# Optimization experiments

Hardware: AMD Instinct MI355X
Metric: run time of the kernel (lower is better)

## Reference

```python
import jax, jax.numpy as jnp
import numpy as np

H = 8  # num heads
LORA_SCALE = 1.0


def _lora(x, down, up):
    # down: [rank, in], up: [out, rank]; sigma_mask is None -> ones -> no-op
    return (x @ down.T) @ up.T


def setup_inputs() -> dict:
    key = jax.random.key(0)
    ks = jax.random.split(key, 16)
    B, S, C = 16, 1024, 1280
    Senc, Cenc = 77, 1024
    rank = 4
    s = lambda n: 1.0 / np.sqrt(n)
    inp = {
        "hidden_states": jax.random.normal(ks[0], (B, S, C), jnp.float32),
        "encoder_hidden_states": jax.random.normal(ks[1], (B, Senc, Cenc), jnp.float32),
        "Wq": jax.random.normal(ks[2], (C, C), jnp.float32) * s(C),
        "Wk": jax.random.normal(ks[3], (C, Cenc), jnp.float32) * s(Cenc),
        "Wv": jax.random.normal(ks[4], (C, Cenc), jnp.float32) * s(Cenc),
        "Wo": jax.random.normal(ks[5], (C, C), jnp.float32) * s(C),
        "bo": jnp.zeros((C,), jnp.float32),
        "q_down": jax.random.normal(ks[6], (rank, C), jnp.float32) / rank,
        "q_up": jax.random.normal(ks[7], (C, rank), jnp.float32) * 0.02,
        "k_down": jax.random.normal(ks[8], (rank, Cenc), jnp.float32) / rank,
        "k_up": jax.random.normal(ks[9], (C, rank), jnp.float32) * 0.02,
        "v_down": jax.random.normal(ks[10], (rank, Cenc), jnp.float32) / rank,
        "v_up": jax.random.normal(ks[11], (C, rank), jnp.float32) * 0.02,
        "o_down": jax.random.normal(ks[12], (rank, C), jnp.float32) / rank,
        "o_up": jax.random.normal(ks[13], (C, rank), jnp.float32) * 0.02,
    }
    return inp


def reference(hidden_states, encoder_hidden_states, Wq, Wk, Wv, Wo, bo,
              q_down, q_up, k_down, k_up, v_down, v_up, o_down, o_up):
    B, S, C = hidden_states.shape
    Senc = encoder_hidden_states.shape[1]
    D = C // H
    attn_scale = 1.0 / jnp.sqrt(jnp.asarray(D, hidden_states.dtype))

    q = hidden_states @ Wq.T + LORA_SCALE * _lora(hidden_states, q_down, q_up)
    k = encoder_hidden_states @ Wk.T + LORA_SCALE * _lora(encoder_hidden_states, k_down, k_up)
    v = encoder_hidden_states @ Wv.T + LORA_SCALE * _lora(encoder_hidden_states, v_down, v_up)

    # head_to_batch_dim: [B, S, H*D] -> [B, H, S, D]
    q = q.reshape(B, S, H, D).transpose(0, 2, 1, 3)
    k = k.reshape(B, Senc, H, D).transpose(0, 2, 1, 3)
    v = v.reshape(B, Senc, H, D).transpose(0, 2, 1, 3)

    scores = jnp.einsum("bhqd,bhkd->bhqk", q, k) * attn_scale
    probs = jax.nn.softmax(scores, axis=-1)
    out = jnp.einsum("bhqk,bhkd->bhqd", probs, v)

    # batch_to_head_dim: [B, H, S, D] -> [B, S, H*D]
    out = out.transpose(0, 2, 1, 3).reshape(B, S, C)
    out = out @ Wo.T + bo + LORA_SCALE * _lora(out, o_down, o_up)
    return out
```

## Files before the change

kernel.cpp:

```cpp
#include <hip/hip_runtime.h>

#define NH    8
#define BB    16
#define SQ    1024
#define CC    1280
#define SENC  77
#define CENC  1024
#define DH    160
#define RANK  4

typedef __attribute__((ext_vector_type(8))) short bf16x8;
typedef __attribute__((ext_vector_type(4))) float f32x4;

__device__ inline void split_bf16(float a, unsigned short& hi, unsigned short& lo) {
    unsigned u = __float_as_uint(a);
    hi = (unsigned short)(u >> 16);
    float fhi = __uint_as_float(u & 0xffff0000u);
    float r = a - fhi;
    lo = (unsigned short)(__float_as_uint(r) >> 16);
}

__global__ void fold_split_kernel(const float* __restrict__ W,
                                  const float* __restrict__ up,
                                  const float* __restrict__ down,
                                  unsigned short* __restrict__ ohi,
                                  unsigned short* __restrict__ olo,
                                  int N, int K) {
    int idx4 = blockIdx.x * blockDim.x + threadIdx.x;
    int total4 = (N * K) >> 2;
    if (idx4 >= total4) return;
    int i = idx4 << 2;
    int n = i / K;
    int kk = i - n * K;
    float4 acc = *(const float4*)(W + i);
#pragma unroll
    for (int r = 0; r < RANK; ++r) {
        float u = up[n * RANK + r];
        float4 dv = *(const float4*)(down + (size_t)r * K + kk);
        acc.x += u * dv.x; acc.y += u * dv.y;
        acc.z += u * dv.z; acc.w += u * dv.w;
    }
    unsigned short h0, h1, h2, h3, l0, l1, l2, l3;
    split_bf16(acc.x, h0, l0); split_bf16(acc.y, h1, l1);
    split_bf16(acc.z, h2, l2); split_bf16(acc.w, h3, l3);
    int2 hv, lv;
    hv.x = (int)((unsigned)h0 | ((unsigned)h1 << 16));
    hv.y = (int)((unsigned)h2 | ((unsigned)h3 << 16));
    lv.x = (int)((unsigned)l0 | ((unsigned)l1 << 16));
    lv.y = (int)((unsigned)l2 | ((unsigned)l3 << 16));
    *(int2*)(ohi + i) = hv;
    *(int2*)(olo + i) = lv;
}

__global__ void fold_split_kv_kernel(const float* __restrict__ Wk,
                                     const float* __restrict__ Wv,
                                     const float* __restrict__ k_up,
                                     const float* __restrict__ k_down,
                                     const float* __restrict__ v_up,
                                     const float* __restrict__ v_down,
                                     unsigned short* __restrict__ ohi,
                                     unsigned short* __restrict__ olo) {
    int idx4 = blockIdx.x * blockDim.x + threadIdx.x;
    int i = idx4 << 2;
    int n = i >> 10;
    int kk = i & 1023;
    const float* W; const float* up; const float* down; int nn = n;
    if (n < CC) { W = Wk; up = k_up; down = k_down; }
    else        { W = Wv; up = v_up; down = v_down; nn = n - CC; }
    float4 acc = *(const float4*)(W + (size_t)nn * CENC + kk);
#pragma unroll
    for (int r = 0; r < RANK; ++r) {
        float u = up[nn * RANK + r];
        float4 dv = *(const float4*)(down + (size_t)r * CENC + kk);
        acc.x += u * dv.x; acc.y += u * dv.y;
        acc.z += u * dv.z; acc.w += u * dv.w;
    }
    unsigned short h0, h1, h2, h3, l0, l1, l2, l3;
    split_bf16(acc.x, h0, l0); split_bf16(acc.y, h1, l1);
    split_bf16(acc.z, h2, l2); split_bf16(acc.w, h3, l3);
    int2 hv, lv;
    hv.x = (int)((unsigned)h0 | ((unsigned)h1 << 16));
    hv.y = (int)((unsigned)h2 | ((unsigned)h3 << 16));
    lv.x = (int)((unsigned)l0 | ((unsigned)l1 << 16));
    lv.y = (int)((unsigned)l2 | ((unsigned)l3 << 16));
    *(int2*)(ohi + i) = hv;
    *(int2*)(olo + i) = lv;
}

__global__ __launch_bounds__(256) void foldT_split_kernel(
    const float* __restrict__ W, const float* __restrict__ up,
    const float* __restrict__ down,
    unsigned short* __restrict__ ohi, unsigned short* __restrict__ olo) {
    __shared__ float t[32][33];
    int tx = threadIdx.x & 31, ty = threadIdx.x >> 5;
    int bx = blockIdx.x, by = blockIdx.y;
    int k = bx * 32 + tx;
#pragma unroll
    for (int r4 = 0; r4 < 4; ++r4) {
        int n = by * 32 + ty + 8 * r4;
        float v = W[(size_t)n * 1280 + k];
#pragma unroll
        for (int r = 0; r < RANK; ++r)
            v += up[n * RANK + r] * down[r * 1280 + k];
        t[ty + 8 * r4][tx] = v;
    }
    __syncthreads();
#pragma unroll
    for (int r4 = 0; r4 < 4; ++r4) {
        float v = t[tx][ty + 8 * r4];
        unsigned short h_, l_;
        split_bf16(v, h_, l_);
        size_t o = (size_t)(bx * 32 + ty + 8 * r4) * 1280 + by * 32 + tx;
        ohi[o] = h_; olo[o] = l_;
    }
}

__global__ void split_kernel(const float* __restrict__ x,
                             unsigned short* __restrict__ ohi,
                             unsigned short* __restrict__ olo, int total4) {
    int idx4 = blockIdx.x * blockDim.x + threadIdx.x;
    if (idx4 >= total4) return;
    int i = idx4 << 2;
    float4 a = *(const float4*)(x + i);
    unsigned short h0, h1, h2, h3, l0, l1, l2, l3;
    split_bf16(a.x, h0, l0); split_bf16(a.y, h1, l1);
    split_bf16(a.z, h2, l2); split_bf16(a.w, h3, l3);
    int2 hv, lv;
    hv.x = (int)((unsigned)h0 | ((unsigned)h1 << 16));
    hv.y = (int)((unsigned)h2 | ((unsigned)h3 << 16));
    lv.x = (int)((unsigned)l0 | ((unsigned)l1 << 16));
    lv.y = (int)((unsigned)l2 | ((unsigned)l3 << 16));
    *(int2*)(ohi + i) = hv;
    *(int2*)(olo + i) = lv;
}

#define GBM 128
#define GBN 128
#define GBK 32

__device__ inline void async_load16(const void* gsrc, void* lds_dst) {
    __builtin_amdgcn_global_load_lds(
        (const __attribute__((address_space(1))) void*)gsrc,
        (__attribute__((address_space(3))) void*)lds_dst, 16, 0, 0);
}

__device__ inline int clampi(int x, int hi) { return x > hi ? hi : x; }

template <int MODE>
__global__ __launch_bounds__(256) void gemm2_kernel(
    const unsigned short* __restrict__ A_hi, const unsigned short* __restrict__ A_lo,
    int lda,
    const unsigned short* __restrict__ W_hi, const unsigned short* __restrict__ W_lo,
    int ldw,
    const float* __restrict__ bias, float* __restrict__ outF,
    unsigned short* __restrict__ oHi, unsigned short* __restrict__ oLo, int ldo,
    int M, int N, int K) {
    __shared__ __align__(16) unsigned short lds[4][GBM][GBK];
    const int tid  = threadIdx.x;
    const int wave = tid >> 6;
    const int lane = tid & 63;

    int m0, n0;
    if constexpr (MODE == 0) {
        n0 = blockIdx.x * GBN; m0 = blockIdx.y * GBM;
    } else if constexpr (MODE == 1) {
        n0 = blockIdx.x * GBN; m0 = 0;
        int z = blockIdx.z, b = z >> 3, hh = z & 7;
        size_t ao = (size_t)(b * SENC) * lda + hh * DH;
        A_hi += ao; A_lo += ao;
        W_hi += hh * DH; W_lo += hh * DH;
        size_t ob = (size_t)(b * 640 + hh * 80) * ldo;
        oHi += ob; oLo += ob;
    } else if constexpr (MODE == 2) {
        n0 = 0; m0 = blockIdx.y * GBM;
        int z = blockIdx.z, b = z >> 3, hh = z & 7;
        A_hi += hh * DH; A_lo += hh * DH;
        size_t wo = (size_t)(b * SENC) * ldw + CC + hh * DH;
        W_hi += wo; W_lo += wo;
        size_t ob = (size_t)b * CC * ldo + hh * 80;
        oHi += ob; oLo += ob;
    } else {
        int bid = blockIdx.x;
        int w = (bid & 7) * 160 + (bid >> 3);
        int mt = w / 10, nt = w - mt * 10;
        m0 = mt * GBM; n0 = nt * GBN;
        int b = m0 >> 10;
        size_t wo = (size_t)b * CC * ldw;
        W_hi += wo; W_lo += wo;
    }

    const int wr = wave >> 1, wc = wave & 1;
    f32x4 zero = {0.f, 0.f, 0.f, 0.f};
    f32x4 acc[4][4];
#pragma unroll
    for (int i = 0; i < 4; ++i)
#pragma unroll
        for (int j = 0; j < 4; ++j) acc[i][j] = zero;

    const int c0 = wave * 2, c1 = wave * 2 + 1;
    const int rr = lane >> 2;
    const int kc = (lane & 3) * 8;
    const int ra0 = clampi(m0 + c0 * 16 + rr, M - 1);
    const int ra1 = clampi(m0 + c1 * 16 + rr, M - 1);
    const int rw0 = clampi(n0 + c0 * 16 + rr, N - 1);
    const int rw1 = clampi(n0 + c1 * 16 + rr, N - 1);
    const unsigned short* pAh0 = A_hi + (size_t)ra0 * lda + kc;
    const unsigned short* pAh1 = A_hi + (size_t)ra1 * lda + kc;
    const unsigned short* pAl0 = A_lo + (size_t)ra0 * lda + kc;
    const unsigned short* pAl1 = A_lo + (size_t)ra1 * lda + kc;
    const unsigned short* pWh0 = W_hi + (size_t)rw0 * ldw + kc;
    const unsigned short* pWh1 = W_hi + (size_t)rw1 * ldw + kc;
    const unsigned short* pWl0 = W_lo + (size_t)rw0 * ldw + kc;
    const unsigned short* pWl1 = W_lo + (size_t)rw1 * ldw + kc;

    for (int k0 = 0; k0 < K; k0 += GBK) {
        async_load16(pAh0 + k0, &lds[0][c0 * 16][0]);
        async_load16(pAh1 + k0, &lds[0][c1 * 16][0]);
        async_load16(pAl0 + k0, &lds[1][c0 * 16][0]);
        async_load16(pAl1 + k0, &lds[1][c1 * 16][0]);
        async_load16(pWh0 + k0, &lds[2][c0 * 16][0]);
        async_load16(pWh1 + k0, &lds[2][c1 * 16][0]);
        async_load16(pWl0 + k0, &lds[3][c0 * 16][0]);
        async_load16(pWl1 + k0, &lds[3][c1 * 16][0]);
        __syncthreads();

        bf16x8 ah[4], al[4], bh[4], bl[4];
        const int fr = lane & 15;
        const int kb = (lane >> 4) * 8;
#pragma unroll
        for (int i = 0; i < 4; ++i) {
            ah[i] = *(const bf16x8*)&lds[0][wr * 64 + i * 16 + fr][kb];
            al[i] = *(const bf16x8*)&lds[1][wr * 64 + i * 16 + fr][kb];
            bh[i] = *(const bf16x8*)&lds[2][wc * 64 + i * 16 + fr][kb];
            bl[i] = *(const bf16x8*)&lds[3][wc * 64 + i * 16 + fr][kb];
        }
#pragma unroll
        for (int i = 0; i < 4; ++i)
#pragma unroll
            for (int j = 0; j < 4; ++j) {
                acc[i][j] = __builtin_amdgcn_mfma_f32_16x16x32_bf16(ah[i], bh[j], acc[i][j], 0, 0, 0);
                acc[i][j] = __builtin_amdgcn_mfma_f32_16x16x32_bf16(ah[i], bl[j], acc[i][j], 0, 0, 0);
                acc[i][j] = __builtin_amdgcn_mfma_f32_16x16x32_bf16(al[i], bh[j], acc[i][j], 0, 0, 0);
            }
        __syncthreads();
    }

    const int fc = lane & 15;
    const int fr4 = (lane >> 4) * 4;
#pragma unroll
    for (int j = 0; j < 4; ++j) {
        int col = n0 + wc * 64 + j * 16 + fc;
        float bv = 0.f;
        if constexpr (MODE == 4) bv = bias[col];
#pragma unroll
        for (int i = 0; i < 4; ++i) {
            int row = m0 + wr * 64 + i * 16 + fr4;
#pragma unroll
            for (int r = 0; r < 4; ++r) {
                int rowr = row + r;
                float val = acc[i][j][r];
                if constexpr (MODE == 0) {
                    if (rowr < M) {
                        unsigned short vh, vl;
                        split_bf16(val, vh, vl);
                        oHi[(size_t)rowr * ldo + col] = vh;
                        oLo[(size_t)rowr * ldo + col] = vl;
                    }
                } else if constexpr (MODE == 1) {
                    if (rowr < 80) {
                        if (rowr >= SENC) val = 0.f;
                        unsigned short vh, vl;
                        split_bf16(val, vh, vl);
                        oHi[(size_t)rowr * ldo + col] = vh;
                        oLo[(size_t)rowr * ldo + col] = vl;
                    }
                } else if constexpr (MODE == 2) {
                    if (col < 80) {
                        if (col >= SENC) val = 0.f;
                        unsigned short vh, vl;
                        split_bf16(val, vh, vl);
                        oHi[(size_t)rowr * ldo + col] = vh;
                        oLo[(size_t)rowr * ldo + col] = vl;
                    }
                } else {
                    outF[(size_t)rowr * ldo + col] = val + bv;
                }
            }
        }
    }
}

__global__ __launch_bounds__(256) void sgemm_softmax_kernel(
    const unsigned short* __restrict__ A_hi, const unsigned short* __restrict__ A_lo,
    const unsigned short* __restrict__ Nbig_hi, const unsigned short* __restrict__ Nbig_lo,
    unsigned short* __restrict__ P_hi, unsigned short* __restrict__ P_lo) {
    __shared__ __align__(16) unsigned short sLDS[18432];
    const int tid = threadIdx.x;
    const int wave = tid >> 6;
    const int lane = tid & 63;
    const int fr = lane & 15;
    const int g = lane >> 4;
    const float scale = 0.07905694150420949f;

    int bid = blockIdx.x;
    int w = (bid & 7) * 64 + (bid >> 3);
    int mt = w >> 2, nt = w & 3;
    const int m0 = mt * 128;
    const int n0 = nt * 160;
    const int b = mt >> 3;
    const unsigned short* W_hi = Nbig_hi + (size_t)b * 640 * CC;
    const unsigned short* W_lo = Nbig_lo + (size_t)b * 640 * CC;

    const int wr = wave >> 1, wc = wave & 1;

    const int rr = lane >> 2;
    const int kcs = ((lane & 3) ^ ((lane >> 3) & 3)) * 8;
    const unsigned short* gsrc[9];
    int ldst[9];
#pragma unroll
    for (int q = 0; q < 9; ++q) {
        int c = wave * 9 + q;
        const unsigned short* base; int ld, row0, toff, lc;
        if (c < 8)       { base = A_hi; ld = CC; row0 = m0; toff = 0;     lc = c; }
        else if (c < 16) { base = A_lo; ld = CC; row0 = m0; toff = 4096;  lc = c - 8; }
        else if (c < 26) { base = W_hi; ld = CC; row0 = n0; toff = 8192;  lc = c - 16; }
        else             { base = W_lo; ld = CC; row0 = n0; toff = 13312; lc = c - 26; }
        gsrc[q] = base + (size_t)(row0 + lc * 16 + rr) * ld + kcs;
        ldst[q] = toff + lc * 512;
    }

    f32x4 zero = {0.f, 0.f, 0.f, 0.f};
    f32x4 acc[4][5];
#pragma unroll
    for (int i = 0; i < 4; ++i)
#pragma unroll
        for (int j = 0; j < 5; ++j) acc[i][j] = zero;

    const int kbsw = (g ^ ((fr >> 1) & 3)) * 8;

    for (int k0 = 0; k0 < CC; k0 += 32) {
#pragma unroll
        for (int q = 0; q < 9; ++q)
            async_load16(gsrc[q] + k0, &sLDS[ldst[q]]);
        __syncthreads();

        bf16x8 ah[4], al[4];
#pragma unroll
        for (int i = 0; i < 4; ++i) {
            int r = wr * 64 + i * 16 + fr;
            ah[i] = *(const bf16x8*)&sLDS[r * 32 + kbsw];
            al[i] = *(const bf16x8*)&sLDS[4096 + r * 32 + kbsw];
        }
#pragma unroll
        for (int j = 0; j < 5; ++j) {
            int rb = wc * 80 + j * 16 + fr;
            bf16x8 bh = *(const bf16x8*)&sLDS[8192 + rb * 32 + kbsw];
            bf16x8 bl = *(const bf16x8*)&sLDS[13312 + rb * 32 + kbsw];
#pragma unroll
            for (int i = 0; i < 4; ++i) {
                acc[i][j] = __builtin_amdgcn_mfma_f32_16x16x32_bf16(ah[i], bh, acc[i][j], 0, 0, 0);
                acc[i][j] = __builtin_amdgcn_mfma_f32_16x16x32_bf16(ah[i], bl, acc[i][j], 0, 0, 0);
                acc[i][j] = __builtin_amdgcn_mfma_f32_16x16x32_bf16(al[i], bh, acc[i][j], 0, 0, 0);
            }
        }
        __syncthreads();
    }

    const int fc = fr;
    const bool maskme = (fc >= 13);
#pragma unroll
    for (int i = 0; i < 4; ++i) {
#pragma unroll
        for (int r = 0; r < 4; ++r) {
            float m = -1e30f;
#pragma unroll
            for (int j = 0; j < 5; ++j) {
                float v = acc[i][j][r] * scale;
                if (j == 4 && maskme) v = -1e30f;
                acc[i][j][r] = v;
                m = fmaxf(m, v);
            }
#pragma unroll
            for (int msk = 1; msk < 16; msk <<= 1) m = fmaxf(m, __shfl_xor(m, msk));
            float sum = 0.f;
#pragma unroll
            for (int j = 0; j < 5; ++j) {
                float e = (j == 4 && maskme) ? 0.f : __expf(acc[i][j][r] - m);
                acc[i][j][r] = e;
                sum += e;
            }
#pragma unroll
            for (int msk = 1; msk < 16; msk <<= 1) sum += __shfl_xor(sum, msk);
            float inv = 1.f / sum;
            int row = m0 + wr * 64 + i * 16 + g * 4 + r;
            size_t ob = (size_t)row * 640 + n0 + wc * 80 + fc;
#pragma unroll
            for (int j = 0; j < 5; ++j) {
                unsigned short ph, pl;
                split_bf16(acc[i][j][r] * inv, ph, pl);
                P_hi[ob + j * 16] = ph;
                P_lo[ob + j * 16] = pl;
            }
        }
    }
}

extern "C" void kernel_launch(void* const* d_in, const int* in_sizes, int n_in,
                              void* d_out, int out_size, void* d_ws, size_t ws_size,
                              hipStream_t stream) {
    const float* hidden = (const float*)d_in[0];
    const float* enc    = (const float*)d_in[1];
    const float* Wq     = (const float*)d_in[2];
    const float* Wk     = (const float*)d_in[3];
    const float* Wv     = (const float*)d_in[4];
    const float* Wo     = (const float*)d_in[5];
    const float* bo     = (const float*)d_in[6];
    const float* q_down = (const float*)d_in[7];
    const float* q_up   = (const float*)d_in[8];
    const float* k_down = (const float*)d_in[9];
    const float* k_up   = (const float*)d_in[10];
    const float* v_down = (const float*)d_in[11];
    const float* v_up   = (const float*)d_in[12];
    const float* o_down = (const float*)d_in[13];
    const float* o_up   = (const float*)d_in[14];

    char* ws = (char*)d_ws;
    unsigned short* Wo_hi   = (unsigned short*)(ws);
    unsigned short* Wo_lo   = (unsigned short*)(ws + 3276800);
    unsigned short* kv_hi   = (unsigned short*)(ws + 6553600);
    unsigned short* kv_lo   = (unsigned short*)(ws + 12861440);
    unsigned short* Wkv_hi  = (unsigned short*)(ws + 19169280);
    unsigned short* Wkv_lo  = (unsigned short*)(ws + 24412160);
    unsigned short* Nbig_hi = (unsigned short*)(ws + 19169280);
    unsigned short* Nbig_lo = (unsigned short*)(ws + 45383680);
    unsigned short* MbT_hi  = (unsigned short*)(ws + 19169280);
    unsigned short* MbT_lo  = (unsigned short*)(ws + 45383680);
    unsigned short* WqT_hi  = (unsigned short*)(ws + 71598080);
    unsigned short* WqT_lo  = (unsigned short*)(ws + 74874880);
    unsigned short* enc_hi  = (unsigned short*)(ws + 78151680);
    unsigned short* enc_lo  = (unsigned short*)(ws + 80674816);
    unsigned short* P_hi    = (unsigned short*)(ws + 78151680);
    unsigned short* P_lo    = (unsigned short*)(ws + 99123200);
    unsigned short* hid_hi  = (unsigned short*)d_out;
    unsigned short* hid_lo  = hid_hi + (size_t)20971520;

    const int M1 = BB * SQ;
    const int M2 = BB * SENC;

    dim3 blk(256);
    fold_split_kernel<<<1600, blk, 0, stream>>>(Wo, o_up, o_down, Wo_hi, Wo_lo, CC, CC);
    foldT_split_kernel<<<dim3(40, 40), blk, 0, stream>>>(Wq, q_up, q_down, WqT_hi, WqT_lo);
    fold_split_kv_kernel<<<2560, blk, 0, stream>>>(Wk, Wv, k_up, k_down, v_up, v_down,
                                                   Wkv_hi, Wkv_lo);
    split_kernel<<<1232, blk, 0, stream>>>(enc, enc_hi, enc_lo, (M2 * CENC) / 4);
    split_kernel<<<20480, blk, 0, stream>>>(hidden, hid_hi, hid_lo, (M1 * CC) / 4);

    gemm2_kernel<0><<<dim3(20, 10), blk, 0, stream>>>(
        enc_hi, enc_lo, CENC, Wkv_hi, Wkv_lo, CENC,
        nullptr, nullptr, kv_hi, kv_lo, 2560, M2, 2560, CENC);

    gemm2_kernel<1><<<dim3(10, 1, 128), blk, 0, stream>>>(
        kv_hi, kv_lo, 2560, WqT_hi, WqT_lo, CC,
        nullptr, nullptr, Nbig_hi, Nbig_lo, CC, SENC, CC, DH);

    sgemm_softmax_kernel<<<512, blk, 0, stream>>>(
        hid_hi, hid_lo, Nbig_hi, Nbig_lo, P_hi, P_lo);

    gemm2_kernel<2><<<dim3(1, 10, 128), blk, 0, stream>>>(
        Wo_hi, Wo_lo, CC, kv_hi, kv_lo, 2560,
        nullptr, nullptr, MbT_hi, MbT_lo, 640, CC, SENC, DH);

    gemm2_kernel<4><<<1280, blk, 0, stream>>>(
        P_hi, P_lo, 640, MbT_hi, MbT_lo, 640,
        bo, (float*)d_out, nullptr, nullptr, CC, M1, CC, 640);
}
```

Measured before the change: 484.7 us.

## Merge prep kernels into one launch and specialize small per-head GEMMs

Replaces five separate fold/split preprocessing launches with a single block-indexed prep kernel that dispatches on block ID. It also replaces the generic 128x128 GEMM used for the per-head Nbig and MbT products with dedicated kernels. These use an 80-row/column tile that matches the 77-length encoder dimension, so fewer MFMAs are wasted on padding. The aim is to cut launch overhead and padded compute on the small GEMMs, at the cost of more specialized code.

```diff
diff --git a/kernel.cpp b/kernel.cpp
--- a/kernel.cpp
+++ b/kernel.cpp
@@ -20,108 +20,8 @@
     lo = (unsigned short)(__float_as_uint(r) >> 16);
 }
 
-__global__ void fold_split_kernel(const float* __restrict__ W,
-                                  const float* __restrict__ up,
-                                  const float* __restrict__ down,
-                                  unsigned short* __restrict__ ohi,
-                                  unsigned short* __restrict__ olo,
-                                  int N, int K) {
-    int idx4 = blockIdx.x * blockDim.x + threadIdx.x;
-    int total4 = (N * K) >> 2;
-    if (idx4 >= total4) return;
-    int i = idx4 << 2;
-    int n = i / K;
-    int kk = i - n * K;
-    float4 acc = *(const float4*)(W + i);
-#pragma unroll
-    for (int r = 0; r < RANK; ++r) {
-        float u = up[n * RANK + r];
-        float4 dv = *(const float4*)(down + (size_t)r * K + kk);
-        acc.x += u * dv.x; acc.y += u * dv.y;
-        acc.z += u * dv.z; acc.w += u * dv.w;
-    }
-    unsigned short h0, h1, h2, h3, l0, l1, l2, l3;
-    split_bf16(acc.x, h0, l0); split_bf16(acc.y, h1, l1);
-    split_bf16(acc.z, h2, l2); split_bf16(acc.w, h3, l3);
-    int2 hv, lv;
-    hv.x = (int)((unsigned)h0 | ((unsigned)h1 << 16));
-    hv.y = (int)((unsigned)h2 | ((unsigned)h3 << 16));
-    lv.x = (int)((unsigned)l0 | ((unsigned)l1 << 16));
-    lv.y = (int)((unsigned)l2 | ((unsigned)l3 << 16));
-    *(int2*)(ohi + i) = hv;
-    *(int2*)(olo + i) = lv;
-}
-
-__global__ void fold_split_kv_kernel(const float* __restrict__ Wk,
-                                     const float* __restrict__ Wv,
-                                     const float* __restrict__ k_up,
-                                     const float* __restrict__ k_down,
-                                     const float* __restrict__ v_up,
-                                     const float* __restrict__ v_down,
-                                     unsigned short* __restrict__ ohi,
-                                     unsigned short* __restrict__ olo) {
-    int idx4 = blockIdx.x * blockDim.x + threadIdx.x;
-    int i = idx4 << 2;
-    int n = i >> 10;
-    int kk = i & 1023;
-    const float* W; const float* up; const float* down; int nn = n;
-    if (n < CC) { W = Wk; up = k_up; down = k_down; }
-    else        { W = Wv; up = v_up; down = v_down; nn = n - CC; }
-    float4 acc = *(const float4*)(W + (size_t)nn * CENC + kk);
-#pragma unroll
-    for (int r = 0; r < RANK; ++r) {
-        float u = up[nn * RANK + r];
-        float4 dv = *(const float4*)(down + (size_t)r * CENC + kk);
-        acc.x += u * dv.x; acc.y += u * dv.y;
-        acc.z += u * dv.z; acc.w += u * dv.w;
-    }
-    unsigned short h0, h1, h2, h3, l0, l1, l2, l3;
-    split_bf16(acc.x, h0, l0); split_bf16(acc.y, h1, l1);
-    split_bf16(acc.z, h2, l2); split_bf16(acc.w, h3, l3);
-    int2 hv, lv;
-    hv.x = (int)((unsigned)h0 | ((unsigned)h1 << 16));
-    hv.y = (int)((unsigned)h2 | ((unsigned)h3 << 16));
-    lv.x = (int)((unsigned)l0 | ((unsigned)l1 << 16));
-    lv.y = (int)((unsigned)l2 | ((unsigned)l3 << 16));
-    *(int2*)(ohi + i) = hv;
-    *(int2*)(olo + i) = lv;
-}
-
-__global__ __launch_bounds__(256) void foldT_split_kernel(
-    const float* __restrict__ W, const float* __restrict__ up,
-    const float* __restrict__ down,
-    unsigned short* __restrict__ ohi, unsigned short* __restrict__ olo) {
-    __shared__ float t[32][33];
-    int tx = threadIdx.x & 31, ty = threadIdx.x >> 5;
-    int bx = blockIdx.x, by = blockIdx.y;
-    int k = bx * 32 + tx;
-#pragma unroll
-    for (int r4 = 0; r4 < 4; ++r4) {
-        int n = by * 32 + ty + 8 * r4;
-        float v = W[(size_t)n * 1280 + k];
-#pragma unroll
-        for (int r = 0; r < RANK; ++r)
-            v += up[n * RANK + r] * down[r * 1280 + k];
-        t[ty + 8 * r4][tx] = v;
-    }
-    __syncthreads();
-#pragma unroll
-    for (int r4 = 0; r4 < 4; ++r4) {
-        float v = t[tx][ty + 8 * r4];
-        unsigned short h_, l_;
-        split_bf16(v, h_, l_);
-        size_t o = (size_t)(bx * 32 + ty + 8 * r4) * 1280 + by * 32 + tx;
-        ohi[o] = h_; olo[o] = l_;
-    }
-}
-
-__global__ void split_kernel(const float* __restrict__ x,
-                             unsigned short* __restrict__ ohi,
-                             unsigned short* __restrict__ olo, int total4) {
-    int idx4 = blockIdx.x * blockDim.x + threadIdx.x;
-    if (idx4 >= total4) return;
-    int i = idx4 << 2;
-    float4 a = *(const float4*)(x + i);
+__device__ inline void split_store4(float4 a, unsigned short* ohi,
+                                    unsigned short* olo, int i) {
     unsigned short h0, h1, h2, h3, l0, l1, l2, l3;
     split_bf16(a.x, h0, l0); split_bf16(a.y, h1, l1);
     split_bf16(a.z, h2, l2); split_bf16(a.w, h3, l3);
@@ -132,6 +32,83 @@
     lv.y = (int)((unsigned)l2 | ((unsigned)l3 << 16));
     *(int2*)(ohi + i) = hv;
     *(int2*)(olo + i) = lv;
+}
+
+__device__ inline float4 fold4(const float* W, const float* up, const float* down,
+                               int n, int kk, int K) {
+    float4 acc = *(const float4*)(W + (size_t)n * K + kk);
+#pragma unroll
+    for (int r = 0; r < RANK; ++r) {
+        float u = up[n * RANK + r];
+        float4 dv = *(const float4*)(down + (size_t)r * K + kk);
+        acc.x += u * dv.x; acc.y += u * dv.y;
+        acc.z += u * dv.z; acc.w += u * dv.w;
+    }
+    return acc;
+}
+
+__global__ __launch_bounds__(256) void prep_kernel(
+    const float* __restrict__ hidden, const float* __restrict__ enc,
+    const float* __restrict__ Wq, const float* __restrict__ Wk,
+    const float* __restrict__ Wv, const float* __restrict__ Wo,
+    const float* __restrict__ q_up, const float* __restrict__ q_down,
+    const float* __restrict__ k_up, const float* __restrict__ k_down,
+    const float* __restrict__ v_up, const float* __restrict__ v_down,
+    const float* __restrict__ o_up, const float* __restrict__ o_down,
+    unsigned short* __restrict__ Wo_hi, unsigned short* __restrict__ Wo_lo,
+    unsigned short* __restrict__ WqT_hi, unsigned short* __restrict__ WqT_lo,
+    unsigned short* __restrict__ Wkv_hi, unsigned short* __restrict__ Wkv_lo,
+    unsigned short* __restrict__ enc_hi, unsigned short* __restrict__ enc_lo,
+    unsigned short* __restrict__ hid_hi, unsigned short* __restrict__ hid_lo) {
+    __shared__ float t[32][33];
+    const int bid = blockIdx.x;
+    const int tid = threadIdx.x;
+
+    if (bid < 1600) {
+        int idx4 = bid * 256 + tid;
+        int i = idx4 << 2;
+        int n = i / CC, kk = i - n * CC;
+        split_store4(fold4(Wo, o_up, o_down, n, kk, CC), Wo_hi, Wo_lo, i);
+    } else if (bid < 3200) {
+        int b2 = bid - 1600;
+        int bx = b2 % 40, by = b2 / 40;
+        int tx = tid & 31, ty = tid >> 5;
+        int k = bx * 32 + tx;
+#pragma unroll
+        for (int r4 = 0; r4 < 4; ++r4) {
+            int n = by * 32 + ty + 8 * r4;
+            float v = Wq[(size_t)n * 1280 + k];
+#pragma unroll
+            for (int r = 0; r < RANK; ++r)
+                v += q_up[n * RANK + r] * q_down[r * 1280 + k];
+            t[ty + 8 * r4][tx] = v;
+        }
+        __syncthreads();
+#pragma unroll
+        for (int r4 = 0; r4 < 4; ++r4) {
+            float v = t[tx][ty + 8 * r4];
+            unsigned short h_, l_;
+            split_bf16(v, h_, l_);
+            size_t o = (size_t)(bx * 32 + ty + 8 * r4) * 1280 + by * 32 + tx;
+            WqT_hi[o] = h_; WqT_lo[o] = l_;
+        }
+    } else if (bid < 5760) {
+        int idx4 = (bid - 3200) * 256 + tid;
+        int i = idx4 << 2;
+        int n = i >> 10, kk = i & 1023;
+        float4 v;
+        if (n < CC) v = fold4(Wk, k_up, k_down, n, kk, CENC);
+        else        v = fold4(Wv, v_up, v_down, n - CC, kk, CENC);
+        split_store4(v, Wkv_hi, Wkv_lo, i);
+    } else if (bid < 6992) {
+        int idx4 = (bid - 5760) * 256 + tid;
+        int i = idx4 << 2;
+        split_store4(*(const float4*)(enc + i), enc_hi, enc_lo, i);
+    } else {
+        int idx4 = (bid - 6992) * 256 + tid;
+        int i = idx4 << 2;
+        split_store4(*(const float4*)(hidden + i), hid_hi, hid_lo, i);
+    }
 }
 
 #define GBM 128
@@ -163,22 +140,6 @@
     int m0, n0;
     if constexpr (MODE == 0) {
         n0 = blockIdx.x * GBN; m0 = blockIdx.y * GBM;
-    } else if constexpr (MODE == 1) {
-        n0 = blockIdx.x * GBN; m0 = 0;
-        int z = blockIdx.z, b = z >> 3, hh = z & 7;
-        size_t ao = (size_t)(b * SENC) * lda + hh * DH;
-        A_hi += ao; A_lo += ao;
-        W_hi += hh * DH; W_lo += hh * DH;
-        size_t ob = (size_t)(b * 640 + hh * 80) * ldo;
-        oHi += ob; oLo += ob;
-    } else if constexpr (MODE == 2) {
-        n0 = 0; m0 = blockIdx.y * GBM;
-        int z = blockIdx.z, b = z >> 3, hh = z & 7;
-        A_hi += hh * DH; A_lo += hh * DH;
-        size_t wo = (size_t)(b * SENC) * ldw + CC + hh * DH;
-        W_hi += wo; W_lo += wo;
-        size_t ob = (size_t)b * CC * ldo + hh * 80;
-        oHi += ob; oLo += ob;
     } else {
         int bid = blockIdx.x;
         int w = (bid & 7) * 160 + (bid >> 3);
@@ -266,28 +227,186 @@
                         oHi[(size_t)rowr * ldo + col] = vh;
                         oLo[(size_t)rowr * ldo + col] = vl;
                     }
-                } else if constexpr (MODE == 1) {
-                    if (rowr < 80) {
-                        if (rowr >= SENC) val = 0.f;
-                        unsigned short vh, vl;
-                        split_bf16(val, vh, vl);
-                        oHi[(size_t)rowr * ldo + col] = vh;
-                        oLo[(size_t)rowr * ldo + col] = vl;
-                    }
-                } else if constexpr (MODE == 2) {
-                    if (col < 80) {
-                        if (col >= SENC) val = 0.f;
-                        unsigned short vh, vl;
-                        split_bf16(val, vh, vl);
-                        oHi[(size_t)rowr * ldo + col] = vh;
-                        oLo[(size_t)rowr * ldo + col] = vl;
-                    }
                 } else {
                     outF[(size_t)rowr * ldo + col] = val + bv;
                 }
             }
         }
     }
+}
+
+__global__ __launch_bounds__(256) void nh_kernel(
+    const unsigned short* __restrict__ kv_hi, const unsigned short* __restrict__ kv_lo,
+    const unsigned short* __restrict__ WqT_hi, const unsigned short* __restrict__ WqT_lo,
+    unsigned short* __restrict__ oHi, unsigned short* __restrict__ oLo) {
+    __shared__ __align__(16) unsigned short sL[13312];
+    const int tid = threadIdx.x, wave = tid >> 6, lane = tid & 63;
+    const int fr = lane & 15, g = lane >> 4, kb = g * 8;
+    const int n0 = blockIdx.x * 128;
+    const int z = blockIdx.y, b = z >> 3, h = z & 7;
+
+    const unsigned short* Abh = kv_hi + (size_t)(b * SENC) * 2560 + h * DH;
+    const unsigned short* Abl = kv_lo + (size_t)(b * SENC) * 2560 + h * DH;
+    const unsigned short* Wbh = WqT_hi + h * DH;
+    const unsigned short* Wbl = WqT_lo + h * DH;
+
+    const int rr = lane >> 2;
+    const int kc = (lane & 3) * 8;
+    const unsigned short* gsrc[7];
+    char* gdst[7];
+    bool gok[7];
+#pragma unroll
+    for (int q = 0; q < 7; ++q) {
+        int c = wave * 7 + q;
+        gok[q] = (c < 26);
+        int cc = gok[q] ? c : 25;
+        const unsigned short* src; int dst;
+        if (cc < 5)       { src = Abh + (size_t)clampi(cc * 16 + rr, 76) * 2560 + kc; dst = cc * 1024; }
+        else if (cc < 10) { src = Abl + (size_t)clampi((cc - 5) * 16 + rr, 76) * 2560 + kc; dst = 5120 + (cc - 5) * 1024; }
+        else if (cc < 18) { src = Wbh + (size_t)(n0 + (cc - 10) * 16 + rr) * 1280 + kc; dst = 10240 + (cc - 10) * 1024; }
+        else              { src = Wbl + (size_t)(n0 + (cc - 18) * 16 + rr) * 1280 + kc; dst = 18432 + (cc - 18) * 1024; }
+        gsrc[q] = src; gdst[q] = (char*)sL + dst;
+    }
+
+    f32x4 zero = {0.f, 0.f, 0.f, 0.f};
+    f32x4 acc[5][2];
+#pragma unroll
+    for (int i = 0; i < 5; ++i)
+#pragma unroll
+        for (int j = 0; j < 2; ++j) acc[i][j] = zero;
+
+    for (int k0 = 0; k0 < DH; k0 += 32) {
+#pragma unroll
+        for (int q = 0; q < 7; ++q)
+            if (gok[q]) async_load16(gsrc[q] + k0, gdst[q]);
+        __syncthreads();
+
+        bf16x8 ah[5], al[5], wh[2], wl[2];
+#pragma unroll
+        for (int i = 0; i < 5; ++i) {
+            ah[i] = *(const bf16x8*)&sL[(i * 16 + fr) * 32 + kb];
+            al[i] = *(const bf16x8*)&sL[2560 + (i * 16 + fr) * 32 + kb];
+        }
+#pragma unroll
+        for (int j = 0; j < 2; ++j) {
+            wh[j] = *(const bf16x8*)&sL[5120 + (wave * 32 + j * 16 + fr) * 32 + kb];
+            wl[j] = *(const bf16x8*)&sL[9216 + (wave * 32 + j * 16 + fr) * 32 + kb];
+        }
+#pragma unroll
+        for (int i = 0; i < 5; ++i)
+#pragma unroll
+            for (int j = 0; j < 2; ++j) {
+                acc[i][j] = __builtin_amdgcn_mfma_f32_16x16x32_bf16(ah[i], wh[j], acc[i][j], 0, 0, 0);
+                acc[i][j] = __builtin_amdgcn_mfma_f32_16x16x32_bf16(ah[i], wl[j], acc[i][j], 0, 0, 0);
+                acc[i][j] = __builtin_amdgcn_mfma_f32_16x16x32_bf16(al[i], wh[j], acc[i][j], 0, 0, 0);
+            }
+        __syncthreads();
+    }
+
+    const int fc = lane & 15;
+    const int fr4 = (lane >> 4) * 4;
+    const size_t obase = (size_t)(b * 640 + h * 80) * 1280;
+#pragma unroll
+    for (int i = 0; i < 5; ++i)
+#pragma unroll
+        for (int j = 0; j < 2; ++j)
+#pragma unroll
+            for (int r = 0; r < 4; ++r) {
+                int row = i * 16 + fr4 + r;
+                int col = n0 + wave * 32 + j * 16 + fc;
+                float v = (row >= SENC) ? 0.f : acc[i][j][r];
+                unsigned short vh, vl;
+                split_bf16(v, vh, vl);
+                oHi[obase + (size_t)row * 1280 + col] = vh;
+                oLo[obase + (size_t)row * 1280 + col] = vl;
+            }
+}
+
+__global__ __launch_bounds__(256) void mh_kernel(
+    const unsigned short* __restrict__ Wo_hi, const unsigned short* __restrict__ Wo_lo,
+    const unsigned short* __restrict__ kv_hi, const unsigned short* __restrict__ kv_lo,
+    unsigned short* __restrict__ oHi, unsigned short* __restrict__ oLo) {
+    __shared__ __align__(16) unsigned short sL[13312];
+    const int tid = threadIdx.x, wave = tid >> 6, lane = tid & 63;
+    const int fr = lane & 15, g = lane >> 4, kb = g * 8;
+    const int m0 = blockIdx.x * 128;
+    const int z = blockIdx.y, b = z >> 3, h = z & 7;
+
+    const unsigned short* Abh = Wo_hi + h * DH;
+    const unsigned short* Abl = Wo_lo + h * DH;
+    const unsigned short* Wbh = kv_hi + (size_t)(b * SENC) * 2560 + CC + h * DH;
+    const unsigned short* Wbl = kv_lo + (size_t)(b * SENC) * 2560 + CC + h * DH;
+
+    const int rr = lane >> 2;
+    const int kc = (lane & 3) * 8;
+    const unsigned short* gsrc[7];
+    char* gdst[7];
+    bool gok[7];
+#pragma unroll
+    for (int q = 0; q < 7; ++q) {
+        int c = wave * 7 + q;
+        gok[q] = (c < 26);
+        int cc = gok[q] ? c : 25;
+        const unsigned short* src; int dst;
+        if (cc < 8)       { src = Abh + (size_t)(m0 + cc * 16 + rr) * 1280 + kc; dst = cc * 1024; }
+        else if (cc < 16) { src = Abl + (size_t)(m0 + (cc - 8) * 16 + rr) * 1280 + kc; dst = 8192 + (cc - 8) * 1024; }
+        else if (cc < 21) { src = Wbh + (size_t)clampi((cc - 16) * 16 + rr, 76) * 2560 + kc; dst = 16384 + (cc - 16) * 1024; }
+        else              { src = Wbl + (size_t)clampi((cc - 21) * 16 + rr, 76) * 2560 + kc; dst = 21504 + (cc - 21) * 1024; }
+        gsrc[q] = src; gdst[q] = (char*)sL + dst;
+    }
+
+    f32x4 zero = {0.f, 0.f, 0.f, 0.f};
+    f32x4 acc[2][5];
+#pragma unroll
+    for (int i = 0; i < 2; ++i)
+#pragma unroll
+        for (int j = 0; j < 5; ++j) acc[i][j] = zero;
+
+    for (int k0 = 0; k0 < DH; k0 += 32) {
+#pragma unroll
+        for (int q = 0; q < 7; ++q)
+            if (gok[q]) async_load16(gsrc[q] + k0, gdst[q]);
+        __syncthreads();
+
+        bf16x8 ah[2], al[2], wh[5], wl[5];
+#pragma unroll
+        for (int i = 0; i < 2; ++i) {
+            ah[i] = *(const bf16x8*)&sL[(wave * 32 + i * 16 + fr) * 32 + kb];
+            al[i] = *(const bf16x8*)&sL[4096 + (wave * 32 + i * 16 + fr) * 32 + kb];
+        }
+#pragma unroll
+        for (int j = 0; j < 5; ++j) {
+            wh[j] = *(const bf16x8*)&sL[8192 + (j * 16 + fr) * 32 + kb];
+            wl[j] = *(const bf16x8*)&sL[10752 + (j * 16 + fr) * 32 + kb];
+        }
+#pragma unroll
+        for (int i = 0; i < 2; ++i)
+#pragma unroll
+            for (int j = 0; j < 5; ++j) {
+                acc[i][j] = __builtin_amdgcn_mfma_f32_16x16x32_bf16(ah[i], wh[j], acc[i][j], 0, 0, 0);
+                acc[i][j] = __builtin_amdgcn_mfma_f32_16x16x32_bf16(ah[i], wl[j], acc[i][j], 0, 0, 0);
+                acc[i][j] = __builtin_amdgcn_mfma_f32_16x16x32_bf16(al[i], wh[j], acc[i][j], 0, 0, 0);
+            }
+        __syncthreads();
+    }
+
+    const int fc = lane & 15;
+    const int fr4 = (lane >> 4) * 4;
+    const size_t obase = (size_t)b * CC * 640 + h * 80;
+#pragma unroll
+    for (int i = 0; i < 2; ++i)
+#pragma unroll
+        for (int j = 0; j < 5; ++j)
+#pragma unroll
+            for (int r = 0; r < 4; ++r) {
+                int row = m0 + wave * 32 + i * 16 + fr4 + r;
+                int col = j * 16 + fc;
+                float v = (col >= SENC) ? 0.f : acc[i][j][r];
+                unsigned short vh, vl;
+                split_bf16(v, vh, vl);
+                oHi[obase + (size_t)row * 640 + col] = vh;
+                oLo[obase + (size_t)row * 640 + col] = vl;
+            }
 }
 
 __global__ __launch_bounds__(256) void sgemm_softmax_kernel(
@@ -448,27 +567,24 @@
     const int M2 = BB * SENC;
 
     dim3 blk(256);
-    fold_split_kernel<<<1600, blk, 0, stream>>>(Wo, o_up, o_down, Wo_hi, Wo_lo, CC, CC);
-    foldT_split_kernel<<<dim3(40, 40), blk, 0, stream>>>(Wq, q_up, q_down, WqT_hi, WqT_lo);
-    fold_split_kv_kernel<<<2560, blk, 0, stream>>>(Wk, Wv, k_up, k_down, v_up, v_down,
-                                                   Wkv_hi, Wkv_lo);
-    split_kernel<<<1232, blk, 0, stream>>>(enc, enc_hi, enc_lo, (M2 * CENC) / 4);
-    split_kernel<<<20480, blk, 0, stream>>>(hidden, hid_hi, hid_lo, (M1 * CC) / 4);
+    prep_kernel<<<27472, blk, 0, stream>>>(
+        hidden, enc, Wq, Wk, Wv, Wo, q_up, q_down, k_up, k_down,
+        v_up, v_down, o_up, o_down,
+        Wo_hi, Wo_lo, WqT_hi, WqT_lo, Wkv_hi, Wkv_lo,
+        enc_hi, enc_lo, hid_hi, hid_lo);
 
     gemm2_kernel<0><<<dim3(20, 10), blk, 0, stream>>>(
         enc_hi, enc_lo, CENC, Wkv_hi, Wkv_lo, CENC,
         nullptr, nullptr, kv_hi, kv_lo, 2560, M2, 2560, CENC);
 
-    gemm2_kernel<1><<<dim3(10, 1, 128), blk, 0, stream>>>(
-        kv_hi, kv_lo, 2560, WqT_hi, WqT_lo, CC,
-        nullptr, nullptr, Nbig_hi, Nbig_lo, CC, SENC, CC, DH);
+    nh_kernel<<<dim3(10, 128), blk, 0, stream>>>(
+        kv_hi, kv_lo, WqT_hi, WqT_lo, Nbig_hi, Nbig_lo);
 
     sgemm_softmax_kernel<<<512, blk, 0, stream>>>(
         hid_hi, hid_lo, Nbig_hi, Nbig_lo, P_hi, P_lo);
 
-    gemm2_kernel<2><<<dim3(1, 10, 128), blk, 0, stream>>>(
-        Wo_hi, Wo_lo, CC, kv_hi, kv_lo, 2560,
-        nullptr, nullptr, MbT_hi, MbT_lo, 640, CC, SENC, DH);
+    mh_kernel<<<dim3(10, 128), blk, 0, stream>>>(
+        Wo_hi, Wo_lo, kv_hi, kv_lo, MbT_hi, MbT_lo);
 
     gemm2_kernel<4><<<1280, blk, 0, stream>>>(
         P_hi, P_lo, 640, MbT_hi, MbT_lo, 640,
```

New measurement: 461.1 us. -4.9%, faster.
